# Performance work log

Measured on AMD Instinct MI355X. Metric: run time of the kernel, lower is better.

Reference implementation:

```python
import jax, jax.numpy as jnp
import numpy as np

CHUNK = 32

def _l2norm(x):
    return x * jax.lax.rsqrt(jnp.sum(x * x, -1, keepdims=True) + 1e-6)

def _short_conv(x, w):
    # x: (B,L,C); depthwise causal conv with kernel w: (C,K), then SiLU
    K = w.shape[-1]; L = x.shape[1]
    xp = jnp.pad(x, ((0, 0), (K - 1, 0), (0, 0)))
    y = sum(xp[:, t:t + L, :] * w[:, t] for t in range(K))
    return jax.nn.silu(y)

def _fir_conv(x, w):
    # x: (B,L,H,D); per-(head,channel) causal FIR, w: (H,D,K)
    B, L, H, D = x.shape; K = w.shape[-1]
    xf = x.reshape(B, L, H * D).transpose(0, 2, 1)          # (B, H*D, L)
    wf = w.reshape(H * D, 1, K)
    y = jax.lax.conv_general_dilated(xf, wf, (1,), [(K - 1, 0)],
                                     feature_group_count=H * D,
                                     dimension_numbers=('NCH', 'OIH', 'NCH'))
    return y.transpose(0, 2, 1).reshape(B, L, H, D)

def _delta_rule(q, k, v, beta, chunk=CHUNK):
    # q,k: (B,H,L,Dk); v: (B,H,L,Dv); beta: (B,H,L)
    B, H, L, Dk = q.shape; Dv = v.shape[-1]
    pad = (-L) % chunk
    if pad:
        q, k, v = (jnp.pad(t, ((0, 0), (0, 0), (0, pad), (0, 0))) for t in (q, k, v))
        beta = jnp.pad(beta, ((0, 0), (0, 0), (0, pad)))
    Lp = L + pad; n = Lp // chunk
    q = _l2norm(q); k = _l2norm(k)
    v = v * beta[..., None]; kb = k * beta[..., None]
    resh = lambda t: t.reshape(B, H, n, chunk, -1)
    q, k, v, kb = map(resh, (q, k, v, kb))
    tri = jnp.triu(jnp.ones((chunk, chunk), bool))       # incl. diagonal
    tri_s = jnp.triu(tri, 1)                              # strict upper
    # iterative inversion of (I + strictly-lower A): A <- A + A@A row-by-row
    A = jnp.where(tri, 0.0, -jnp.einsum('bhncd,bhnmd->bhncm', kb, k))
    for i in range(1, chunk):
        A = A.at[..., i, :i].add(jnp.einsum('...j,...jk->...k', A[..., i, :], A[..., :, :i]))
    T = A + jnp.eye(chunk, dtype=A.dtype)
    u = T @ v                                             # (B,H,n,c,Dv)
    w = T @ kb                                            # (B,H,n,c,Dk)
    def step(S, inp):
        qi, ki, ui, wi = inp
        attn = jnp.where(tri_s, 0.0, qi @ jnp.swapaxes(ki, -1, -2))
        u_i = ui - wi @ S
        o = qi @ S + attn @ u_i
        S = S + jnp.swapaxes(ki, -1, -2) @ u_i
        return S, o
    S0 = jnp.zeros((B, H, Dk, Dv), q.dtype)
    blocks = lambda t: jnp.moveaxis(t, 2, 0)
    S, out = jax.lax.scan(step, S0, (blocks(q), blocks(k), blocks(u), blocks(w)))
    out = jnp.moveaxis(out, 0, 2).reshape(B, H, Lp, Dv)[:, :, :L]
    return out, S

def setup_inputs():
    key = jax.random.key(0)
    B, L, D, H = 2, 2048, 1024, 4
    Dv = D // H
    ks = jax.random.split(key, 16)
    nrm = lambda k, s, sc: jax.random.normal(k, s, jnp.float32) * sc
    gate_in_dim = D + 2 * H * 4
    hid = 2 * D
    return {
        'hidden_states': nrm(ks[0], (B, L, D), 1.0),
        'Wq': nrm(ks[1], (D, D), D ** -0.5),
        'Wk': nrm(ks[2], (D, D), D ** -0.5),
        'Wv': nrm(ks[3], (D, D), D ** -0.5),
        'Wb': nrm(ks[4], (H, D), D ** -0.5),
        'qconv_w': nrm(ks[5], (D, 4), 0.5),
        'kconv_w': nrm(ks[6], (D, 4), 0.5),
        'vconv_w': nrm(ks[7], (D, 4), 0.5),
        'fir_short_w': jnp.zeros((H, Dv, 3)).at[..., -1].set(1.0) + nrm(ks[8], (H, Dv, 3), 0.02),
        'fir_long_w': jnp.zeros((H, Dv, 63)).at[..., -1].set(1.0) + nrm(ks[9], (H, Dv, 63), 0.02),
        'gate_w1': nrm(ks[10], (hid, gate_in_dim), gate_in_dim ** -0.5),
        'gate_b1': jnp.zeros((hid,), jnp.float32),
        'gate_w2': nrm(ks[11], (H * 4, hid), hid ** -0.5),
        'log_temp': jnp.zeros((H,), jnp.float32),
        'base_bias': jnp.zeros((H, 4)).at[:, 3].set(2.0),
        'floor_raw': jnp.full((H, 4), float(np.log(0.5)), jnp.float32),
        'onorm_w': jnp.ones((Dv,), jnp.float32),
        'Wo': nrm(ks[12], (D, D), D ** -0.5),
    }

def reference(hidden_states, Wq, Wk, Wv, Wb, qconv_w, kconv_w, vconv_w,
              fir_short_w, fir_long_w, gate_w1, gate_b1, gate_w2,
              log_temp, base_bias, floor_raw, onorm_w, Wo):
    B, L, D = hidden_states.shape
    H = log_temp.shape[0]; P = 4
    q = _short_conv(hidden_states @ Wq.T, qconv_w).reshape(B, L, H, -1)
    k = _short_conv(hidden_states @ Wk.T, kconv_w).reshape(B, L, H, -1)
    v = _short_conv(hidden_states @ Wv.T, vconv_w).reshape(B, L, H, -1)
    beta = jax.nn.sigmoid(hidden_states @ Wb.T)          # (B,L,H)
    tr = lambda t: jnp.swapaxes(t, 1, 2)
    delta, _S = _delta_rule(tr(q), tr(k), tr(v), jnp.swapaxes(beta, 1, 2))
    delta = jnp.swapaxes(delta, 1, 2)                    # (B,L,H,Dv)
    short = _fir_conv(v, fir_short_w)
    longp = _fir_conv(v, fir_long_w)
    paths = (short, longp, delta, v)
    def stats(p):
        m = p.mean(-1); va = p.var(-1)
        return jnp.stack([m, va], -1).reshape(B, L, H * 2)
    gate_in = jnp.concatenate([hidden_states] + [stats(p) for p in paths], -1)
    hmid = jax.nn.gelu(gate_in @ gate_w1.T + gate_b1, approximate=False)
    logits = hmid @ gate_w2.T + base_bias.reshape(-1)
    temp = jax.nn.softplus(log_temp) + 1e-4
    logits = logits.reshape(B, L, H, P) / temp[None, None, :, None]
    probs = jax.nn.softmax(logits, -1)
    floor_val = 0.05 * jax.nn.sigmoid(floor_raw)         # floor_mag at step 0 == floor_start
    probs = jnp.maximum(probs, floor_val)
    probs = probs / probs.sum(-1, keepdims=True)
    out = sum(probs[..., i, None] * p for i, p in enumerate(paths))
    out = out * jax.lax.rsqrt(jnp.mean(out * out, -1, keepdims=True) + 1e-5) * onorm_w
    return out.reshape(B, L, -1) @ Wo.T
```

## Files before the change

kernel.cpp:

```cpp
#include <hip/hip_runtime.h>
#include <cmath>

typedef __bf16 bf16;
typedef __bf16 bf16x8 __attribute__((ext_vector_type(8)));
typedef float  f32x4  __attribute__((ext_vector_type(4)));

#define MFMA16(a, b, c) __builtin_amdgcn_mfma_f32_16x16x32_bf16(a, b, c, 0, 0, 0)

#define GLD16(gsrc, ldst)                                                     \
  __builtin_amdgcn_global_load_lds(                                           \
      (const __attribute__((address_space(1))) unsigned*)(gsrc),              \
      (__attribute__((address_space(3))) unsigned*)(ldst), 16, 0, 0)

static __device__ __forceinline__ unsigned pack2(float a, float b) {
  unsigned short ua = __builtin_bit_cast(unsigned short, (__bf16)a);
  unsigned short ub = __builtin_bit_cast(unsigned short, (__bf16)b);
  return (unsigned)ua | ((unsigned)ub << 16);
}

__global__ __launch_bounds__(256)
void kcvt(const float* __restrict__ in, bf16* __restrict__ outp, int n) {
  int i = (blockIdx.x * 256 + threadIdx.x) * 8;
  if (i < n) {
    float4 a = *(const float4*)(in + i);
    float4 b = *(const float4*)(in + i + 4);
    uint4 v = make_uint4(pack2(a.x, a.y), pack2(a.z, a.w),
                         pack2(b.x, b.y), pack2(b.z, b.w));
    *(uint4*)(outp + i) = v;
  }
}

__global__ __launch_bounds__(256)
void kcvt_pad(const float* __restrict__ in, bf16* __restrict__ outp,
              int cin, int cout) {
  int r = blockIdx.x, c = threadIdx.x * 8;
  if (c >= cout) return;
  uint4 v = make_uint4(0u, 0u, 0u, 0u);
  if (c < cin) {
    float4 a = *(const float4*)(in + (size_t)r * cin + c);
    float4 b = *(const float4*)(in + (size_t)r * cin + c + 4);
    v = make_uint4(pack2(a.x, a.y), pack2(a.z, a.w),
                   pack2(b.x, b.y), pack2(b.z, b.w));
  }
  *(uint4*)(outp + (size_t)r * cout + c) = v;
}

template<int EPI>
__global__ __launch_bounds__(256)
void gemm_bf16(const bf16* __restrict__ A, const bf16* __restrict__ Bt,
               const float* __restrict__ bias, float* __restrict__ C,
               int M, int N, int K) {
  __shared__ __align__(16) bf16 sA[2][128 * 64];
  __shared__ __align__(16) bf16 sB[2][128 * 64];
  const int t = threadIdx.x;
  const int w = t >> 6, l = t & 63, lr = l & 15, lg = l >> 4;
  const int m0 = blockIdx.y * 128, n0 = blockIdx.x * 128;
  const int wm = (w & 1) * 64, wn = (w >> 1) * 64;
  const int w32 = w * 32;
  const int nst = K >> 6;

  f32x4 acc[4][4];
#pragma unroll
  for (int mt = 0; mt < 4; ++mt)
#pragma unroll
    for (int nt = 0; nt < 4; ++nt) acc[mt][nt] = (f32x4){0.f, 0.f, 0.f, 0.f};

  auto stage = [&](int s, int bf) {
    const char* ga = (const char*)A + ((size_t)(m0 + w32) * K + (size_t)s * 64) * 2;
    const char* gb = (const char*)Bt + ((size_t)(n0 + w32) * K + (size_t)s * 64) * 2;
    char* da = (char*)&sA[bf][0] + w32 * 128;
    char* db = (char*)&sB[bf][0] + w32 * 128;
    const size_t rs = (size_t)K * 2;
#pragma unroll
    for (int i = 0; i < 4; ++i) {
      GLD16(ga + (i * 8 + (l >> 3)) * rs + (l & 7) * 16, da + i * 1024);
      GLD16(gb + (i * 8 + (l >> 3)) * rs + (l & 7) * 16, db + i * 1024);
    }
  };

  stage(0, 0);
  __syncthreads();
  for (int s = 0; s < nst; ++s) {
    const int bf = s & 1;
    if (s + 1 < nst) stage(s + 1, bf ^ 1);
    const char* pa = (const char*)&sA[bf][0];
    const char* pb = (const char*)&sB[bf][0];
#pragma unroll
    for (int kb = 0; kb < 2; ++kb) {
      bf16x8 af[4], bfg[4];
#pragma unroll
      for (int mt = 0; mt < 4; ++mt)
        af[mt] = *(const bf16x8*)(pa + (wm + mt * 16 + lr) * 128 + kb * 64 + lg * 16);
#pragma unroll
      for (int nt = 0; nt < 4; ++nt)
        bfg[nt] = *(const bf16x8*)(pb + (wn + nt * 16 + lr) * 128 + kb * 64 + lg * 16);
#pragma unroll
      for (int mt = 0; mt < 4; ++mt)
#pragma unroll
        for (int nt = 0; nt < 4; ++nt)
          acc[mt][nt] = MFMA16(af[mt], bfg[nt], acc[mt][nt]);
    }
    __syncthreads();
  }

#pragma unroll
  for (int mt = 0; mt < 4; ++mt)
#pragma unroll
    for (int nt = 0; nt < 4; ++nt) {
      int nn = n0 + wn + nt * 16 + lr;
#pragma unroll
      for (int j = 0; j < 4; ++j) {
        int m = m0 + wm + mt * 16 + lg * 4 + j;
        float x = acc[mt][nt][j];
        if (EPI == 1) {
          x += bias[nn];
          x = 0.5f * x * (1.f + erff(x * 0.70710678118654752f));
        }
        C[(size_t)m * N + nn] = x;
      }
    }
}

__global__ __launch_bounds__(256)
void k2_conv(const float* __restrict__ hs, const float* __restrict__ qkv,
             const float* __restrict__ qw, const float* __restrict__ kw,
             const float* __restrict__ vw, const float* __restrict__ Wb,
             float* __restrict__ qn, float* __restrict__ kn,
             float* __restrict__ vpath, float* __restrict__ beta) {
  const int bid  = blockIdx.x;
  const int b    = bid >> 11;
  const int l    = bid & 2047;
  const int t    = threadIdx.x;
  const int wv   = t >> 6;
  const int lane = t & 63;
  const size_t row = (size_t)bid;

  __shared__ float s_red[4][4];

  float pb[4] = {0.f, 0.f, 0.f, 0.f};
#pragma unroll
  for (int i = 0; i < 4; ++i) {
    int c = wv * 256 + lane + i * 64;
    float x = hs[row * 1024 + c];
    pb[0] += x * Wb[0 * 1024 + c];
    pb[1] += x * Wb[1 * 1024 + c];
    pb[2] += x * Wb[2 * 1024 + c];
    pb[3] += x * Wb[3 * 1024 + c];
  }
#pragma unroll
  for (int off = 32; off; off >>= 1) {
    pb[0] += __shfl_xor(pb[0], off);
    pb[1] += __shfl_xor(pb[1], off);
    pb[2] += __shfl_xor(pb[2], off);
    pb[3] += __shfl_xor(pb[3], off);
  }
  if (lane == 0) {
    s_red[0][wv] = pb[0]; s_red[1][wv] = pb[1];
    s_red[2][wv] = pb[2]; s_red[3][wv] = pb[3];
  }
  __syncthreads();

  float xq[4], xk[4], xv[4];
#pragma unroll
  for (int i = 0; i < 4; ++i) {
    int c = wv * 256 + lane + i * 64;
    float aq = 0.f, ak = 0.f, av = 0.f;
#pragma unroll
    for (int j = 0; j < 4; ++j) {
      int ls = l - 3 + j;
      if (ls >= 0) {
        size_t ro = (size_t)(b * 2048 + ls) * 3072 + c;
        aq = fmaf(qkv[ro], qw[c * 4 + j], aq);
        ak = fmaf(qkv[ro + 1024], kw[c * 4 + j], ak);
        av = fmaf(qkv[ro + 2048], vw[c * 4 + j], av);
      }
    }
    xq[i] = aq / (1.f + expf(-aq));
    xk[i] = ak / (1.f + expf(-ak));
    xv[i] = av / (1.f + expf(-av));
  }

  float sq = 0.f, sk = 0.f;
#pragma unroll
  for (int i = 0; i < 4; ++i) { sq += xq[i] * xq[i]; sk += xk[i] * xk[i]; }
#pragma unroll
  for (int off = 32; off; off >>= 1) {
    sq += __shfl_xor(sq, off);
    sk += __shfl_xor(sk, off);
  }
  float rq = rsqrtf(sq + 1e-6f);
  float rk = rsqrtf(sk + 1e-6f);
  float bsum = s_red[wv][0] + s_red[wv][1] + s_red[wv][2] + s_red[wv][3];
  float betaw = 1.f / (1.f + expf(-bsum));
  if (lane == 0) beta[(size_t)bid * 4 + wv] = betaw;

  const int chk = l >> 5, pos = l & 31;
  size_t cbase = ((size_t)((b * 4 + wv) * 64 + chk) * 32 + pos) * 256;
#pragma unroll
  for (int i = 0; i < 4; ++i) {
    int d = lane + i * 64;
    qn[cbase + d] = xq[i] * rq;
    kn[cbase + d] = xk[i] * rk;
    vpath[row * 1024 + wv * 256 + d] = xv[i];
  }
}

__global__ __launch_bounds__(256)
void k3_chunk(const float* __restrict__ qn, const float* __restrict__ kn,
              const float* __restrict__ vpath, const float* __restrict__ beta,
              float* __restrict__ u, bf16* __restrict__ qb,
              bf16* __restrict__ wb, bf16* __restrict__ knTp,
              bf16* __restrict__ attnb) {
  __shared__ float s_kn[32][257];
  __shared__ float s_kb[32][257];
  __shared__ float s_x[32][257];
  __shared__ float s_A[32][33];
  __shared__ float s_beta[32];
  const int bid = blockIdx.x;
  const int bh = bid >> 6, chk = bid & 63;
  const int b = bh >> 2, h = bh & 3;
  const int t = threadIdx.x;
  const size_t base = (size_t)bid * 8192;

  if (t < 32)
    s_beta[t] = beta[((size_t)(b * 2048 + chk * 32 + t)) * 4 + h];
  for (int i = 0; i < 32; ++i) {
    int idx = t + i * 256;
    int r = idx >> 8, d = idx & 255;
    s_kn[r][d] = kn[base + idx];
    s_x[r][d]  = qn[base + idx];
  }
  __syncthreads();
  for (int i = 0; i < 32; ++i) {
    int idx = t + i * 256;
    int r = idx >> 8, d = idx & 255;
    s_kb[r][d] = s_kn[r][d] * s_beta[r];
  }
  __syncthreads();

  {
    const int r = t & 31, cg = t >> 5;
    float accA[4] = {0.f, 0.f, 0.f, 0.f};
    float accT[4] = {0.f, 0.f, 0.f, 0.f};
    for (int d = 0; d < 256; ++d) {
      float kbr = s_kb[r][d];
      float qr  = s_x[r][d];
#pragma unroll
      for (int q = 0; q < 4; ++q) {
        float knc = s_kn[cg * 4 + q][d];
        accA[q] = fmaf(kbr, knc, accA[q]);
        accT[q] = fmaf(qr,  knc, accT[q]);
      }
    }
    float at[4];
#pragma unroll
    for (int q = 0; q < 4; ++q) {
      int c = cg * 4 + q;
      s_A[r][c] = (r > c) ? -accA[q] : 0.f;
      at[q] = (r >= c) ? accT[q] : 0.f;
    }
    uint2 pk2;
    pk2.x = pack2(at[0], at[1]);
    pk2.y = pack2(at[2], at[3]);
    *(uint2*)((char*)attnb + (size_t)bid * 2048 +
              ((r >> 4) * 64 + (cg >> 1) * 16 + (r & 15)) * 16 + (cg & 1) * 8) = pk2;
  }

  for (int i = 0; i < 32; ++i) {
    int idx = t + i * 256;
    int r = idx >> 8, d = idx & 255;
    *(bf16*)((char*)qb + (size_t)bid * 16384 + r * 512 +
             ((2 * d) ^ ((r & 15) << 4))) = (bf16)s_x[r][d];
  }
  for (int i = 0; i < 32; ++i) {
    int d = (i << 3) + (t >> 5);
    int r = t & 31;
    knTp[(size_t)bid * 8192 + d * 32 + r] = (bf16)s_kn[r][d];
  }
  __syncthreads();

  for (int i = 1; i < 32; ++i) {
    float s = 0.f;
    if (t < i) {
      for (int j = 0; j < 32; ++j) s = fmaf(s_A[i][j], s_A[j][t], s);
    }
    __syncthreads();
    if (t < i) s_A[i][t] += s;
    __syncthreads();
  }

  for (int i = 0; i < 32; ++i) {
    int idx = t + i * 256;
    int r = idx >> 8, d = idx & 255;
    s_x[r][d] = vpath[((size_t)(b * 2048 + chk * 32 + r)) * 1024 + h * 256 + d]
                * s_beta[r];
  }
  __syncthreads();

  {
    const int lane = t & 63, wvv = t >> 6;
    for (int rr = 0; rr < 8; ++rr) {
      int r = wvv * 8 + rr;
      float au[4] = {0.f, 0.f, 0.f, 0.f};
      float aw[4] = {0.f, 0.f, 0.f, 0.f};
      for (int j = 0; j <= r; ++j) {
        float tc = (j == r) ? 1.f : s_A[r][j];
#pragma unroll
        for (int dd = 0; dd < 4; ++dd) {
          au[dd] = fmaf(tc, s_x[j][lane + dd * 64], au[dd]);
          aw[dd] = fmaf(tc, s_kb[j][lane + dd * 64], aw[dd]);
        }
      }
#pragma unroll
      for (int dd = 0; dd < 4; ++dd) {
        int d = lane + dd * 64;
        u[(size_t)bid * 8192 + (d >> 4) * 512 + (r >> 4) * 256 +
          ((((r >> 2) & 3) << 4) + (d & 15)) * 4 + (r & 3)] = au[dd];
        *(bf16*)((char*)wb + (size_t)bid * 16384 + r * 512 +
                 ((2 * d) ^ ((r & 15) << 4))) = (bf16)(-aw[dd]);
      }
    }
  }
}

__global__ __launch_bounds__(64, 1)
void k4_scan_mfma(const bf16* __restrict__ qb, const bf16* __restrict__ wbp,
                  const bf16* __restrict__ knTp, const bf16* __restrict__ attnb,
                  const float* __restrict__ u, float* __restrict__ delta) {
  __shared__ __align__(16) bf16 s_w[2][32 * 256];
  __shared__ __align__(16) bf16 s_q[2][32 * 256];
  __shared__ __align__(16) bf16 s_kT[2][256 * 32];
  __shared__ __align__(16) float s_u[2][512];
  __shared__ __align__(16) bf16 s_at[2][1024];
  __shared__ __align__(16) bf16 s_S[16 * 264];
  __shared__ __align__(16) bf16 s_tT[16 * 40];
  const int l = threadIdx.x;
  const int lr = l & 15, lg = l >> 4;
  const int bh = blockIdx.x & 7;
  const int slice = blockIdx.x >> 3;
  const int b = bh >> 2, h = bh & 3;
  const int chb = bh * 64;

  for (int i = l; i < 16 * 264 / 2; i += 64) ((unsigned*)s_S)[i] = 0u;
  f32x4 S[16];
#pragma unroll
  for (int dt = 0; dt < 16; ++dt) S[dt] = (f32x4){0.f, 0.f, 0.f, 0.f};

  auto stage = [&](int ck, int bf) {
    const char* gw = (const char*)wbp  + (size_t)ck * 16384;
    const char* gq = (const char*)qb   + (size_t)ck * 16384;
    const char* gk = (const char*)knTp + (size_t)ck * 16384;
    const char* gu = (const char*)u + (size_t)ck * 32768 + slice * 2048;
    const char* ga = (const char*)attnb + (size_t)ck * 2048;
    char* dw = (char*)&s_w[bf][0];
    char* dq = (char*)&s_q[bf][0];
    char* dk = (char*)&s_kT[bf][0];
    char* du = (char*)&s_u[bf][0];
    char* da = (char*)&s_at[bf][0];
#pragma unroll
    for (int i = 0; i < 16; ++i) GLD16(gw + i * 1024 + l * 16, dw + i * 1024);
#pragma unroll
    for (int i = 0; i < 16; ++i) GLD16(gq + i * 1024 + l * 16, dq + i * 1024);
#pragma unroll
    for (int i = 0; i < 16; ++i) GLD16(gk + i * 1024 + l * 16, dk + i * 1024);
#pragma unroll
    for (int i = 0; i < 2; ++i)  GLD16(gu + i * 1024 + l * 16, du + i * 1024);
#pragma unroll
    for (int i = 0; i < 2; ++i)  GLD16(ga + i * 1024 + l * 16, da + i * 1024);
  };

  stage(chb, 0);
  asm volatile("s_waitcnt vmcnt(0)" ::: "memory");
  __builtin_amdgcn_sched_barrier(0);

#pragma clang loop unroll(disable)
  for (int t = 0; t < 64; ++t) {
    const int bc = t & 1;
    asm volatile("s_waitcnt vmcnt(0)" ::: "memory");
    __builtin_amdgcn_sched_barrier(0);
    if (t < 63) stage(chb + t + 1, bc ^ 1);

    const char* pw = (const char*)&s_w[bc][0];
    const char* pq = (const char*)&s_q[bc][0];
    f32x4 t0 = *(const f32x4*)(&s_u[bc][0] + l * 4);
    f32x4 t1 = *(const f32x4*)(&s_u[bc][0] + 256 + l * 4);
    bf16x8 atA0 = *(const bf16x8*)((const char*)&s_at[bc][0] + l * 16);
    bf16x8 atA1 = *(const bf16x8*)((const char*)&s_at[bc][0] + 1024 + l * 16);
    f32x4 o0 = (f32x4){0.f, 0.f, 0.f, 0.f};
    f32x4 o1 = (f32x4){0.f, 0.f, 0.f, 0.f};
#pragma unroll
    for (int kb = 0; kb < 8; ++kb) {
      const int sw = (kb * 64 + lg * 16) ^ (lr << 4);
      bf16x8 sB  = *(const bf16x8*)((const char*)s_S + lr * 528 + kb * 64 + lg * 16);
      bf16x8 aw0 = *(const bf16x8*)(pw + lr * 512 + sw);
      bf16x8 aw1 = *(const bf16x8*)(pw + (16 + lr) * 512 + sw);
      bf16x8 aq0 = *(const bf16x8*)(pq + lr * 512 + sw);
      bf16x8 aq1 = *(const bf16x8*)(pq + (16 + lr) * 512 + sw);
      t0 = MFMA16(aw0, sB, t0);
      t1 = MFMA16(aw1, sB, t1);
      o0 = MFMA16(aq0, sB, o0);
      o1 = MFMA16(aq1, sB, o1);
    }
    *(unsigned*)((char*)s_tT + lr * 80 + lg * 8)          = pack2(t0[0], t0[1]);
    *(unsigned*)((char*)s_tT + lr * 80 + lg * 8 + 4)      = pack2(t0[2], t0[3]);
    *(unsigned*)((char*)s_tT + lr * 80 + 32 + lg * 8)     = pack2(t1[0], t1[1]);
    *(unsigned*)((char*)s_tT + lr * 80 + 32 + lg * 8 + 4) = pack2(t1[2], t1[3]);

    bf16x8 tB = *(const bf16x8*)((const char*)s_tT + lr * 80 + lg * 16);
    o0 = MFMA16(atA0, tB, o0);
    o1 = MFMA16(atA1, tB, o1);
    {
      size_t col = h * 256 + slice * 16 + lr;
#pragma unroll
      for (int j = 0; j < 4; ++j) {
        int r0 = t * 32 + lg * 4 + j;
        delta[((size_t)(b * 2048 + r0)) * 1024 + col] = o0[j];
        delta[((size_t)(b * 2048 + r0 + 16)) * 1024 + col] = o1[j];
      }
    }

    const char* pk = (const char*)&s_kT[bc][0];
#pragma unroll
    for (int dt = 0; dt < 16; ++dt) {
      bf16x8 aK = *(const bf16x8*)(pk + (dt * 16 + lr) * 64 + lg * 16);
      S[dt] = MFMA16(aK, tB, S[dt]);
    }
#pragma unroll
    for (int dt = 0; dt < 16; ++dt) {
      *(unsigned*)((char*)s_S + lr * 528 + dt * 32 + lg * 8)     = pack2(S[dt][0], S[dt][1]);
      *(unsigned*)((char*)s_S + lr * 528 + dt * 32 + lg * 8 + 4) = pack2(S[dt][2], S[dt][3]);
    }
  }
}

__global__ __launch_bounds__(256)
void k5_fir(const float* __restrict__ vpath, const float* __restrict__ wsrt,
            const float* __restrict__ wlng, float* __restrict__ shortp,
            float* __restrict__ longp) {
  __shared__ float s_v[126][128];
  const int c0 = blockIdx.x * 128;
  const int l0 = blockIdx.y * 64;
  const int b  = blockIdx.z;
  const int t  = threadIdx.x;

  for (int i = 0; i < 63; ++i) {
    int idx = t + i * 256;
    int rr = idx >> 7, cc2 = idx & 127;
    int gl = l0 - 62 + rr;
    s_v[rr][cc2] = (gl >= 0)
        ? vpath[((size_t)(b * 2048 + gl)) * 1024 + c0 + cc2] : 0.f;
  }

  const int cc = t & 127, lh = t >> 7;
  float wl[63];
#pragma unroll
  for (int j = 0; j < 63; ++j)
    wl[j] = wlng[(size_t)(c0 + cc) * 63 + j];
  float ws0 = wsrt[(size_t)(c0 + cc) * 3 + 0];
  float ws1 = wsrt[(size_t)(c0 + cc) * 3 + 1];
  float ws2 = wsrt[(size_t)(c0 + cc) * 3 + 2];
  __syncthreads();

  for (int m = 0; m < 32; ++m) {
    int ll = lh * 32 + m;
    float accL = 0.f;
#pragma unroll
    for (int j = 0; j < 63; ++j)
      accL = fmaf(s_v[ll + j][cc], wl[j], accL);
    float accS = s_v[ll + 60][cc] * ws0;
    accS = fmaf(s_v[ll + 61][cc], ws1, accS);
    accS = fmaf(s_v[ll + 62][cc], ws2, accS);
    size_t o = ((size_t)(b * 2048 + l0 + ll)) * 1024 + c0 + cc;
    longp[o] = accL;
    shortp[o] = accS;
  }
}

__global__ __launch_bounds__(256)
void k6_gatein(const float* __restrict__ hs, const float* __restrict__ shortp,
               const float* __restrict__ longp, const float* __restrict__ delta,
               const float* __restrict__ vpath, bf16* __restrict__ gate_in) {
  const size_t row = blockIdx.x;
  const int t = threadIdx.x, wv = t >> 6, lane = t & 63;
  bf16* gr = gate_in + row * 1088;
#pragma unroll
  for (int i = 0; i < 2; ++i) {
    int c2 = (t + i * 256) * 2;
    float a = hs[row * 1024 + c2];
    float b = hs[row * 1024 + c2 + 1];
    *(unsigned*)(gr + c2) = pack2(a, b);
  }
  if (t < 16) *(unsigned*)(gr + 1056 + t * 2) = 0u;
  const float* paths[4] = {shortp, longp, delta, vpath};
#pragma unroll
  for (int p = 0; p < 4; ++p) {
    float s = 0.f, sq = 0.f;
#pragma unroll
    for (int i = 0; i < 4; ++i) {
      int c = wv * 256 + lane + i * 64;
      float x = paths[p][row * 1024 + c];
      s += x; sq += x * x;
    }
#pragma unroll
    for (int off = 32; off; off >>= 1) {
      s += __shfl_xor(s, off);
      sq += __shfl_xor(sq, off);
    }
    if (lane == 0) {
      float mean = s * (1.f / 256.f);
      float var = sq * (1.f / 256.f) - mean * mean;
      *(unsigned*)(gr + 1024 + p * 8 + wv * 2) = pack2(mean, var);
    }
  }
}

__global__ __launch_bounds__(256)
void k8_probs(const float* __restrict__ hmid, const float* __restrict__ w2,
              const float* __restrict__ bias, const float* __restrict__ log_temp,
              const float* __restrict__ floor_raw, float* __restrict__ probs) {
  const int t = threadIdx.x, wv = t >> 6, lane = t & 63;
  const size_t row = (size_t)blockIdx.x * 4 + wv;
  float acc[16];
#pragma unroll
  for (int o = 0; o < 16; ++o) acc[o] = 0.f;
  for (int it = 0; it < 32; ++it) {
    int c = lane + it * 64;
    float x = hmid[row * 2048 + c];
#pragma unroll
    for (int o = 0; o < 16; ++o)
      acc[o] = fmaf(x, w2[o * 2048 + c], acc[o]);
  }
#pragma unroll
  for (int off = 32; off; off >>= 1)
#pragma unroll
    for (int o = 0; o < 16; ++o) acc[o] += __shfl_xor(acc[o], off);

  if (lane == 0) {
    for (int h2 = 0; h2 < 4; ++h2) {
      float temp = log1pf(expf(log_temp[h2])) + 1e-4f;
      float li[4], m = -1e30f;
#pragma unroll
      for (int p = 0; p < 4; ++p) {
        li[p] = (acc[h2 * 4 + p] + bias[h2 * 4 + p]) / temp;
        m = fmaxf(m, li[p]);
      }
      float sum = 0.f;
#pragma unroll
      for (int p = 0; p < 4; ++p) { li[p] = expf(li[p] - m); sum += li[p]; }
      float pr[4], s2 = 0.f;
#pragma unroll
      for (int p = 0; p < 4; ++p) {
        float fv = 0.05f / (1.f + expf(-floor_raw[h2 * 4 + p]));
        pr[p] = fmaxf(li[p] / sum, fv);
        s2 += pr[p];
      }
#pragma unroll
      for (int p = 0; p < 4; ++p)
        probs[row * 16 + h2 * 4 + p] = pr[p] / s2;
    }
  }
}

__global__ __launch_bounds__(256)
void k9_mix(const float* __restrict__ shortp, const float* __restrict__ longp,
            const float* __restrict__ delta, const float* __restrict__ vpath,
            const float* __restrict__ probs, const float* __restrict__ onorm,
            bf16* __restrict__ mixed) {
  const size_t row = blockIdx.x;
  const int t = threadIdx.x, wv = t >> 6, lane = t & 63;
  float p0 = probs[row * 16 + wv * 4 + 0];
  float p1 = probs[row * 16 + wv * 4 + 1];
  float p2 = probs[row * 16 + wv * 4 + 2];
  float p3 = probs[row * 16 + wv * 4 + 3];
  float m[4];
  float sq = 0.f;
#pragma unroll
  for (int i = 0; i < 4; ++i) {
    int c = wv * 256 + lane + i * 64;
    size_t o = row * 1024 + c;
    float x = p0 * shortp[o] + p1 * longp[o] + p2 * delta[o] + p3 * vpath[o];
    m[i] = x;
    sq += x * x;
  }
#pragma unroll
  for (int off = 32; off; off >>= 1) sq += __shfl_xor(sq, off);
  float sc = rsqrtf(sq * (1.f / 256.f) + 1e-5f);
#pragma unroll
  for (int i = 0; i < 4; ++i) {
    int d = lane + i * 64;
    mixed[row * 1024 + wv * 256 + d] = (bf16)(m[i] * sc * onorm[d]);
  }
}

extern "C" void kernel_launch(void* const* d_in, const int* in_sizes, int n_in,
                              void* d_out, int out_size, void* d_ws,
                              size_t ws_size, hipStream_t stream) {
  const float* hs   = (const float*)d_in[0];
  const float* Wq   = (const float*)d_in[1];
  const float* Wk   = (const float*)d_in[2];
  const float* Wv   = (const float*)d_in[3];
  const float* Wb   = (const float*)d_in[4];
  const float* qw   = (const float*)d_in[5];
  const float* kw   = (const float*)d_in[6];
  const float* vw   = (const float*)d_in[7];
  const float* fsw  = (const float*)d_in[8];
  const float* flw  = (const float*)d_in[9];
  const float* gw1  = (const float*)d_in[10];
  const float* gb1  = (const float*)d_in[11];
  const float* gw2  = (const float*)d_in[12];
  const float* ltmp = (const float*)d_in[13];
  const float* bbias= (const float*)d_in[14];
  const float* frw  = (const float*)d_in[15];
  const float* onw  = (const float*)d_in[16];
  const float* Wo   = (const float*)d_in[17];
  float* out = (float*)d_out;

  float* f = (float*)d_ws;
  const size_t BLD = 4194304;
  float* qkv     = f + 0 * BLD;
  float* qn      = f + 3 * BLD;
  float* kn      = f + 4 * BLD;
  float* vpath   = f + 5 * BLD;
  float* shortp  = f + 6 * BLD;
  float* longp   = f + 7 * BLD;
  float* gate_f  = f + 8 * BLD;
  float* probs   = gate_f + 4325376;
  float* beta    = probs + 65536;

  bf16* hsb  = (bf16*)gate_f;
  bf16* ginb = (bf16*)gate_f;
  bf16* gw1b = (bf16*)gate_f + 4456448;
  bf16* wob  = (bf16*)gate_f + 4456448 + 2228224;
  bf16* wqb  = (bf16*)kn;
  bf16* wkb  = wqb + 1048576;
  bf16* wvb  = wkb + 1048576;

  float* u_f32 = f + 0 * BLD;
  bf16*  qbb   = (bf16*)shortp;
  bf16*  wbb   = qbb + 512 * 8192;
  bf16*  knTb  = (bf16*)longp;
  bf16*  attnb = knTb + 512 * 8192;
  float* delta = f + 2 * BLD;
  float* hmid  = qn;
  bf16*  mixb  = (bf16*)(f + 1 * BLD);

  kcvt<<<2048, 256, 0, stream>>>(hs, hsb, 4194304);
  kcvt<<<512, 256, 0, stream>>>(Wq, wqb, 1048576);
  kcvt<<<512, 256, 0, stream>>>(Wk, wkb, 1048576);
  kcvt<<<512, 256, 0, stream>>>(Wv, wvb, 1048576);
  kcvt<<<512, 256, 0, stream>>>(Wo, wob, 1048576);
  kcvt_pad<<<2048, 256, 0, stream>>>(gw1, gw1b, 1056, 1088);

  gemm_bf16<0><<<dim3(24, 32), 256, 0, stream>>>(hsb, wqb, nullptr, qkv, 4096, 3072, 1024);

  k2_conv<<<4096, 256, 0, stream>>>(hs, qkv, qw, kw, vw, Wb,
                                    qn, kn, vpath, beta);
  k3_chunk<<<512, 256, 0, stream>>>(qn, kn, vpath, beta, u_f32, qbb, wbb,
                                    knTb, attnb);
  k4_scan_mfma<<<128, 64, 0, stream>>>(qbb, wbb, knTb, attnb, u_f32, delta);
  k5_fir<<<dim3(8, 32, 2), 256, 0, stream>>>(vpath, fsw, flw, shortp, longp);
  k6_gatein<<<4096, 256, 0, stream>>>(hs, shortp, longp, delta, vpath, ginb);
  gemm_bf16<1><<<dim3(16, 32), 256, 0, stream>>>(ginb, gw1b, gb1, hmid, 4096, 2048, 1088);
  k8_probs<<<1024, 256, 0, stream>>>(hmid, gw2, bbias, ltmp, frw, probs);
  k9_mix<<<4096, 256, 0, stream>>>(shortp, longp, delta, vpath, probs, onw, mixb);
  gemm_bf16<0><<<dim3(8, 32), 256, 0, stream>>>(mixb, wob, nullptr, out, 4096, 1024, 1024);
}
```

Measured before the change: 607.8 us.

## Move chunk-prep matmuls in k3_chunk onto bf16 MFMA and merge weight conversions

k3_chunk now stages q, k and beta-scaled k in swizzled bf16 shared memory. It computes the kb·kᵀ and q·kᵀ products and the T·v and T·kb products with 16x16x32 bf16 MFMA instructions, replacing scalar FMA loops. The triangular inversion runs in a single wave without block-wide barriers, and shared memory is shrunk so two blocks can fit per CU. The four weight conversion launches are merged into one kernel. In exchange, A, T, u and w are now computed from bf16 operands, where they were previously computed in fp32.

```diff
diff --git a/kernel.cpp b/kernel.cpp
--- a/kernel.cpp
+++ b/kernel.cpp
@@ -28,6 +28,22 @@
                          pack2(b.x, b.y), pack2(b.z, b.w));
     *(uint4*)(outp + i) = v;
   }
+}
+
+__global__ __launch_bounds__(256)
+void kcvt4(const float* __restrict__ i0, const float* __restrict__ i1,
+           const float* __restrict__ i2, const float* __restrict__ i3,
+           bf16* __restrict__ o0, bf16* __restrict__ o1,
+           bf16* __restrict__ o2, bf16* __restrict__ o3) {
+  int seg = blockIdx.x >> 9;
+  int i = (((blockIdx.x & 511) * 256) + threadIdx.x) * 8;
+  const float* in = (seg == 0) ? i0 : (seg == 1) ? i1 : (seg == 2) ? i2 : i3;
+  bf16* outp = (seg == 0) ? o0 : (seg == 1) ? o1 : (seg == 2) ? o2 : o3;
+  float4 a = *(const float4*)(in + i);
+  float4 b = *(const float4*)(in + i + 4);
+  uint4 v = make_uint4(pack2(a.x, a.y), pack2(a.z, a.w),
+                       pack2(b.x, b.y), pack2(b.z, b.w));
+  *(uint4*)(outp + i) = v;
 }
 
 __global__ __launch_bounds__(256)
@@ -205,119 +221,134 @@
   }
 }
 
-__global__ __launch_bounds__(256)
+__global__ __launch_bounds__(256, 2)
 void k3_chunk(const float* __restrict__ qn, const float* __restrict__ kn,
               const float* __restrict__ vpath, const float* __restrict__ beta,
               float* __restrict__ u, bf16* __restrict__ qb,
               bf16* __restrict__ wb, bf16* __restrict__ knTp,
               bf16* __restrict__ attnb) {
-  __shared__ float s_kn[32][257];
-  __shared__ float s_kb[32][257];
-  __shared__ float s_x[32][257];
-  __shared__ float s_A[32][33];
-  __shared__ float s_beta[32];
+  __shared__ __align__(16) char sm[64256];
+  bf16* s_knb = (bf16*)(sm);
+  bf16* s_qbt = (bf16*)(sm + 16384);
+  bf16* s_kbb = (bf16*)(sm + 32768);
+  bf16* s_kbT = (bf16*)(sm + 16384);
+  bf16* s_vbT = (bf16*)(sm + 36864);
+  bf16* s_T   = (bf16*)(sm + 57344);
+  float (*s_A)[33] = (float(*)[33])(sm + 59904);
+  float* s_beta = (float*)(sm + 64128);
+
   const int bid = blockIdx.x;
   const int bh = bid >> 6, chk = bid & 63;
   const int b = bh >> 2, h = bh & 3;
   const int t = threadIdx.x;
+  const int w = t >> 6, l = t & 63, lr = l & 15, lg = l >> 4;
   const size_t base = (size_t)bid * 8192;
 
   if (t < 32)
     s_beta[t] = beta[((size_t)(b * 2048 + chk * 32 + t)) * 4 + h];
+  __syncthreads();
+
+  float vv[32], kbr[32];
+#pragma unroll
   for (int i = 0; i < 32; ++i) {
-    int idx = t + i * 256;
-    int r = idx >> 8, d = idx & 255;
-    s_kn[r][d] = kn[base + idx];
-    s_x[r][d]  = qn[base + idx];
-  }
-  __syncthreads();
-  for (int i = 0; i < 32; ++i) {
-    int idx = t + i * 256;
-    int r = idx >> 8, d = idx & 255;
-    s_kb[r][d] = s_kn[r][d] * s_beta[r];
-  }
-  __syncthreads();
-
-  {
-    const int r = t & 31, cg = t >> 5;
-    float accA[4] = {0.f, 0.f, 0.f, 0.f};
-    float accT[4] = {0.f, 0.f, 0.f, 0.f};
-    for (int d = 0; d < 256; ++d) {
-      float kbr = s_kb[r][d];
-      float qr  = s_x[r][d];
-#pragma unroll
-      for (int q = 0; q < 4; ++q) {
-        float knc = s_kn[cg * 4 + q][d];
-        accA[q] = fmaf(kbr, knc, accA[q]);
-        accT[q] = fmaf(qr,  knc, accT[q]);
-      }
-    }
-    float at[4];
-#pragma unroll
-    for (int q = 0; q < 4; ++q) {
-      int c = cg * 4 + q;
-      s_A[r][c] = (r > c) ? -accA[q] : 0.f;
-      at[q] = (r >= c) ? accT[q] : 0.f;
-    }
-    uint2 pk2;
-    pk2.x = pack2(at[0], at[1]);
-    pk2.y = pack2(at[2], at[3]);
-    *(uint2*)((char*)attnb + (size_t)bid * 2048 +
-              ((r >> 4) * 64 + (cg >> 1) * 16 + (r & 15)) * 16 + (cg & 1) * 8) = pk2;
-  }
-
-  for (int i = 0; i < 32; ++i) {
-    int idx = t + i * 256;
-    int r = idx >> 8, d = idx & 255;
-    *(bf16*)((char*)qb + (size_t)bid * 16384 + r * 512 +
-             ((2 * d) ^ ((r & 15) << 4))) = (bf16)s_x[r][d];
-  }
+    float qv = qn[base + i * 256 + t];
+    float kv = kn[base + i * 256 + t];
+    float be = s_beta[i];
+    vv[i]  = vpath[((size_t)(b * 2048 + chk * 32 + i)) * 1024 + h * 256 + t] * be;
+    kbr[i] = kv * be;
+    const int sw = (2 * t) ^ ((i & 15) << 4);
+    *(bf16*)((char*)s_knb + i * 512 + sw) = (bf16)kv;
+    *(bf16*)((char*)s_qbt + i * 512 + sw) = (bf16)qv;
+    *(bf16*)((char*)s_kbb + i * 512 + sw) = (bf16)kbr[i];
+    *(bf16*)((char*)qb + (size_t)bid * 16384 + i * 512 + sw) = (bf16)qv;
+  }
+  __syncthreads();
+
+#pragma unroll
   for (int i = 0; i < 32; ++i) {
     int d = (i << 3) + (t >> 5);
     int r = t & 31;
-    knTp[(size_t)bid * 8192 + d * 32 + r] = (bf16)s_kn[r][d];
-  }
-  __syncthreads();
-
-  for (int i = 1; i < 32; ++i) {
-    float s = 0.f;
-    if (t < i) {
-      for (int j = 0; j < 32; ++j) s = fmaf(s_A[i][j], s_A[j][t], s);
-    }
-    __syncthreads();
-    if (t < i) s_A[i][t] += s;
-    __syncthreads();
-  }
-
-  for (int i = 0; i < 32; ++i) {
-    int idx = t + i * 256;
-    int r = idx >> 8, d = idx & 255;
-    s_x[r][d] = vpath[((size_t)(b * 2048 + chk * 32 + r)) * 1024 + h * 256 + d]
-                * s_beta[r];
-  }
-  __syncthreads();
-
+    bf16 kv = *(const bf16*)((char*)s_knb + r * 512 + ((2 * d) ^ ((r & 15) << 4)));
+    knTp[base + d * 32 + r] = kv;
+  }
   {
-    const int lane = t & 63, wvv = t >> 6;
-    for (int rr = 0; rr < 8; ++rr) {
-      int r = wvv * 8 + rr;
-      float au[4] = {0.f, 0.f, 0.f, 0.f};
-      float aw[4] = {0.f, 0.f, 0.f, 0.f};
-      for (int j = 0; j <= r; ++j) {
-        float tc = (j == r) ? 1.f : s_A[r][j];
-#pragma unroll
-        for (int dd = 0; dd < 4; ++dd) {
-          au[dd] = fmaf(tc, s_x[j][lane + dd * 64], au[dd]);
-          aw[dd] = fmaf(tc, s_kb[j][lane + dd * 64], aw[dd]);
-        }
+    const int am = w & 1, an = w >> 1;
+    f32x4 accA = (f32x4){0.f, 0.f, 0.f, 0.f};
+    f32x4 accT = (f32x4){0.f, 0.f, 0.f, 0.f};
+#pragma unroll
+    for (int kb = 0; kb < 8; ++kb) {
+      const int swz = (kb * 64 + lg * 16) ^ (lr << 4);
+      bf16x8 aKB = *(const bf16x8*)((char*)s_kbb + (am * 16 + lr) * 512 + swz);
+      bf16x8 aQ  = *(const bf16x8*)((char*)s_qbt + (am * 16 + lr) * 512 + swz);
+      bf16x8 bKN = *(const bf16x8*)((char*)s_knb + (an * 16 + lr) * 512 + swz);
+      accA = MFMA16(aKB, bKN, accA);
+      accT = MFMA16(aQ,  bKN, accT);
+    }
+#pragma unroll
+    for (int j = 0; j < 4; ++j) {
+      int R = am * 16 + lg * 4 + j, C = an * 16 + lr;
+      s_A[R][C] = (R > C) ? -accA[j] : 0.f;
+      float at = (R >= C) ? accT[j] : 0.f;
+      *(bf16*)((char*)attnb + (size_t)bid * 2048 + am * 1024 +
+               ((lg * 4 + j) + ((C >> 3) << 4)) * 16 + (C & 7) * 2) = (bf16)at;
+    }
+  }
+  __syncthreads();
+
+  if (w == 0) {
+    for (int i = 1; i < 32; ++i) {
+      float s = 0.f;
+      if (l < i) {
+        for (int j = 0; j < 32; ++j) s = fmaf(s_A[i][j], s_A[j][l], s);
+        s_A[i][l] += s;
       }
-#pragma unroll
-      for (int dd = 0; dd < 4; ++dd) {
-        int d = lane + dd * 64;
-        u[(size_t)bid * 8192 + (d >> 4) * 512 + (r >> 4) * 256 +
-          ((((r >> 2) & 3) << 4) + (d & 15)) * 4 + (r & 3)] = au[dd];
-        *(bf16*)((char*)wb + (size_t)bid * 16384 + r * 512 +
-                 ((2 * d) ^ ((r & 15) << 4))) = (bf16)(-aw[dd]);
+    }
+  }
+#pragma unroll
+  for (int i = 0; i < 32; i += 2) {
+    *(unsigned*)((char*)s_vbT + t * 80 + i * 2) = pack2(vv[i], vv[i + 1]);
+    *(unsigned*)((char*)s_kbT + t * 80 + i * 2) = pack2(kbr[i], kbr[i + 1]);
+  }
+  __syncthreads();
+
+  {
+    int r = t >> 3, c0 = (t & 7) * 4;
+    float v0 = (r == c0)     ? 1.f : (r > c0     ? s_A[r][c0]     : 0.f);
+    float v1 = (r == c0 + 1) ? 1.f : (r > c0 + 1 ? s_A[r][c0 + 1] : 0.f);
+    float v2 = (r == c0 + 2) ? 1.f : (r > c0 + 2 ? s_A[r][c0 + 2] : 0.f);
+    float v3 = (r == c0 + 3) ? 1.f : (r > c0 + 3 ? s_A[r][c0 + 3] : 0.f);
+    *(unsigned*)((char*)s_T + r * 80 + c0 * 2)     = pack2(v0, v1);
+    *(unsigned*)((char*)s_T + r * 80 + c0 * 2 + 4) = pack2(v2, v3);
+  }
+  __syncthreads();
+
+  {
+    bf16x8 aT0 = *(const bf16x8*)((char*)s_T + lr * 80 + lg * 16);
+    bf16x8 aT1 = *(const bf16x8*)((char*)s_T + (16 + lr) * 80 + lg * 16);
+#pragma unroll
+    for (int nt = 0; nt < 4; ++nt) {
+      const int n = w * 4 + nt;
+      bf16x8 bV = *(const bf16x8*)((char*)s_vbT + (n * 16 + lr) * 80 + lg * 16);
+      bf16x8 bK = *(const bf16x8*)((char*)s_kbT + (n * 16 + lr) * 80 + lg * 16);
+      f32x4 u0 = (f32x4){0.f, 0.f, 0.f, 0.f};
+      f32x4 u1 = (f32x4){0.f, 0.f, 0.f, 0.f};
+      f32x4 w0 = (f32x4){0.f, 0.f, 0.f, 0.f};
+      f32x4 w1 = (f32x4){0.f, 0.f, 0.f, 0.f};
+      u0 = MFMA16(aT0, bV, u0);
+      u1 = MFMA16(aT1, bV, u1);
+      w0 = MFMA16(aT0, bK, w0);
+      w1 = MFMA16(aT1, bK, w1);
+      *(f32x4*)((char*)u + (size_t)bid * 32768 + n * 2048 + l * 16)        = u0;
+      *(f32x4*)((char*)u + (size_t)bid * 32768 + n * 2048 + 1024 + l * 16) = u1;
+#pragma unroll
+      for (int j = 0; j < 4; ++j) {
+        int C = n * 16 + lr;
+        int R0 = lg * 4 + j;
+        int R1 = 16 + lg * 4 + j;
+        *(bf16*)((char*)wb + (size_t)bid * 16384 + R0 * 512 +
+                 ((2 * C) ^ ((R0 & 15) << 4))) = (bf16)(-w0[j]);
+        *(bf16*)((char*)wb + (size_t)bid * 16384 + R1 * 512 +
+                 ((2 * C) ^ ((R1 & 15) << 4))) = (bf16)(-w1[j]);
       }
     }
   }
@@ -645,10 +676,7 @@
   bf16*  mixb  = (bf16*)(f + 1 * BLD);
 
   kcvt<<<2048, 256, 0, stream>>>(hs, hsb, 4194304);
-  kcvt<<<512, 256, 0, stream>>>(Wq, wqb, 1048576);
-  kcvt<<<512, 256, 0, stream>>>(Wk, wkb, 1048576);
-  kcvt<<<512, 256, 0, stream>>>(Wv, wvb, 1048576);
-  kcvt<<<512, 256, 0, stream>>>(Wo, wob, 1048576);
+  kcvt4<<<2048, 256, 0, stream>>>(Wq, Wk, Wv, Wo, wqb, wkb, wvb, wob);
   kcvt_pad<<<2048, 256, 0, stream>>>(gw1, gw1b, 1056, 1088);
 
   gemm_bf16<0><<<dim3(24, 32), 256, 0, stream>>>(hsb, wqb, nullptr, qkv, 4096, 3072, 1024);
```

After: 552.8 us. 9.0% less time.
